# Kernel tuning notes

Hardware: AMD Instinct MI355X
Metric: run time of the kernel (lower is better)

The kernel has to match this reference:

```python
import jax, jax.numpy as jnp
import numpy as np

N = 100000          # atoms
E = 3200000         # edges (avg degree 32)
G = 2000            # molecules in batch
HID = 64            # hidden_channels == num_filters
NG = 50             # num_gaussians
CUTOFF = 10.0
LOG2 = float(np.log(2.0))


def ssp(x):
    # shifted softplus: softplus(x) - log(2)
    return jax.nn.softplus(x) - LOG2


def setup_inputs() -> dict:
    key = jax.random.key(0)
    ks = jax.random.split(key, 24)
    z = jax.random.randint(ks[0], (N,), 0, 100)
    pos = jax.random.uniform(ks[1], (N, 3), dtype=jnp.float32) * 5.0  # distances < cutoff
    batch = jnp.sort(jax.random.randint(ks[2], (N,), 0, G))
    edge_index = jax.random.randint(ks[3], (2, E), 0, N)

    def w(k, *shape):
        fan_in = shape[0]
        return jax.random.normal(k, shape, dtype=jnp.float32) / jnp.sqrt(jnp.float32(fan_in))

    emb = jax.random.normal(ks[4], (100, HID), dtype=jnp.float32)
    L = 3  # num_interactions; stack per-layer params on leading axis
    params = {
        'mlp_w1': w(ks[5], NG, HID)[None].repeat(L, 0) * 0 + jnp.stack([w(jax.random.fold_in(ks[5], i), NG, HID) for i in range(L)]),
        'mlp_b1': jnp.zeros((L, HID), jnp.float32),
        'mlp_w2': jnp.stack([w(jax.random.fold_in(ks[6], i), HID, HID) for i in range(L)]),
        'mlp_b2': jnp.zeros((L, HID), jnp.float32),
        'cf_lin1_w': jnp.stack([w(jax.random.fold_in(ks[7], i), HID, HID) for i in range(L)]),  # no bias
        'cf_lin2_w': jnp.stack([w(jax.random.fold_in(ks[8], i), HID, HID) for i in range(L)]),
        'cf_lin2_b': jnp.zeros((L, HID), jnp.float32),
        'int_lin_w': jnp.stack([w(jax.random.fold_in(ks[9], i), HID, HID) for i in range(L)]),
        'int_lin_b': jnp.zeros((L, HID), jnp.float32),
    }
    out_w1 = w(ks[10], HID, HID // 2)
    out_b1 = jnp.zeros((HID // 2,), jnp.float32)
    out_w2 = w(ks[11], HID // 2, 1)
    out_b2 = jnp.zeros((1,), jnp.float32)
    fin_w = w(ks[12], 1, 1)
    fin_b = jnp.zeros((1,), jnp.float32)
    return dict(z=z, pos=pos, batch=batch, edge_index=edge_index, emb=emb,
                out_w1=out_w1, out_b1=out_b1, out_w2=out_w2, out_b2=out_b2,
                fin_w=fin_w, fin_b=fin_b, **params)


def reference(z, pos, batch, edge_index, emb,
              mlp_w1, mlp_b1, mlp_w2, mlp_b2,
              cf_lin1_w, cf_lin2_w, cf_lin2_b,
              int_lin_w, int_lin_b,
              out_w1, out_b1, out_w2, out_b2, fin_w, fin_b):
    src, dst = edge_index[0], edge_index[1]
    h = emb[z]                                   # [N, 64]
    # edge distances
    d = jnp.linalg.norm(pos[src] - pos[dst], axis=-1)        # [E]
    # Gaussian smearing
    offsets = jnp.linspace(0.0, CUTOFF, NG, dtype=jnp.float32)
    delta = offsets[1] - offsets[0]
    coeff = -0.5 / (delta * delta)
    rbf = jnp.exp(coeff * (d[:, None] - offsets) ** 2)       # [E, 50]
    # cosine cutoff
    C = 0.5 * (jnp.cos(d * (jnp.pi / CUTOFF)) + 1.0)         # [E]

    L = mlp_w1.shape[0]
    for l in range(L):  # small fixed number of interaction blocks
        W = ssp(rbf @ mlp_w1[l] + mlp_b1[l]) @ mlp_w2[l] + mlp_b2[l]  # [E, 64]
        W = W * C[:, None]
        x = h @ cf_lin1_w[l]                                  # [N, 64]
        msg = x[src] * W                                      # [E, 64]
        agg = jax.ops.segment_sum(msg, dst, num_segments=N)   # [N, 64]
        x = agg @ cf_lin2_w[l] + cf_lin2_b[l]
        x = ssp(x)
        x = x @ int_lin_w[l] + int_lin_b[l]
        h = h + x

    h = ssp(h @ out_w1 + out_b1) @ out_w2 + out_b2            # [N, 1]
    out = jax.ops.segment_sum(h, batch, num_segments=G)       # [G, 1]
    return out @ fin_w + fin_b                                # trailing Linear(1,1)
```

## Files before the change

kernel.cpp:

```cpp
#include <hip/hip_runtime.h>
#include <hip/hip_fp16.h>
#include <cstdint>
#include <cstddef>

#define HIDC   64
#define NGAUSS 50
#define NLAYER 3
#define TGRID  8192
#define BSTRIDE 128
#define MAXBUCK 1024
#define CHUNK_E 6656
#define CUTOFF_F 10.0f
#define LOG2_C 0.69314718055994530942f

typedef _Float16 f16x8 __attribute__((ext_vector_type(8)));
typedef float f32x4 __attribute__((ext_vector_type(4)));
#define MFMA16(a, b, c) __builtin_amdgcn_mfma_f32_16x16x32_f16(a, b, c, 0, 0, 0)

__device__ __forceinline__ float sspf(float v) {
  return fmaxf(v, 0.0f) + log1pf(expf(-fabsf(v))) - LOG2_C;
}

__global__ __launch_bounds__(64) void build_table_k(
    const float* __restrict__ mlp_w1, const float* __restrict__ mlp_b1,
    const float* __restrict__ mlp_w2, const float* __restrict__ mlp_b2,
    __half* __restrict__ tabh) {
  int pid = blockIdx.x;
  int l = pid / TGRID;
  int g = pid - l * TGRID;
  int j = threadIdx.x;
  float d = (float)g * (CUTOFF_F / (float)(TGRID - 1));
  __shared__ float rbf_s[NGAUSS];
  __shared__ float hid_s[HIDC];
  const float delta = CUTOFF_F / (float)(NGAUSS - 1);
  const float coeff = -0.5f / (delta * delta);
  if (j < NGAUSS) {
    float t = d - (float)j * delta;
    rbf_s[j] = expf(coeff * t * t);
  }
  __syncthreads();
  const float* w1 = mlp_w1 + (size_t)l * NGAUSS * HIDC;
  float acc = mlp_b1[l * HIDC + j];
#pragma unroll
  for (int k = 0; k < NGAUSS; ++k) acc = fmaf(rbf_s[k], w1[k * HIDC + j], acc);
  hid_s[j] = sspf(acc);
  __syncthreads();
  const float* w2 = mlp_w2 + (size_t)l * HIDC * HIDC;
  float acc2 = mlp_b2[l * HIDC + j];
#pragma unroll
  for (int m = 0; m < HIDC; ++m) acc2 = fmaf(hid_s[m], w2[m * HIDC + j], acc2);
  float C = 0.5f * (cosf(d * (3.14159265358979323846f / CUTOFF_F)) + 1.0f);
  tabh[(size_t)pid * HIDC + j] = __float2half(acc2 * C);
}

__global__ __launch_bounds__(64) void pack_all_k(
    const float* __restrict__ cf1, const float* __restrict__ cf2,
    const float* __restrict__ intw, const float* __restrict__ ow1,
    __half* __restrict__ wpk) {
  int m = blockIdx.x;
  int lane = threadIdx.x;
  const float* src;
  int nc = 64;
  if (m < 3)      src = cf1 + (size_t)m * 4096;
  else if (m < 6) src = cf2 + (size_t)(m - 3) * 4096;
  else if (m < 9) src = intw + (size_t)(m - 6) * 4096;
  else          { src = ow1; nc = 32; }
  __half* dst = wpk + (size_t)m * 4096;
  for (int ct = 0; ct < nc / 16; ++ct)
    for (int kh = 0; kh < 2; ++kh)
      for (int j = 0; j < 8; ++j)
        dst[((ct * 2 + kh) * 64 + lane) * 8 + j] =
            __float2half(src[(kh * 32 + (lane >> 4) * 8 + j) * nc +
                             ct * 16 + (lane & 15)]);
}

__global__ __launch_bounds__(256) void chist_k(
    const int* __restrict__ edst, int* __restrict__ chunk_hist,
    int* __restrict__ bcnt, int E, int nbuck) {
  __shared__ int cnt[MAXBUCK];
  for (int i = threadIdx.x; i < MAXBUCK; i += 256) cnt[i] = 0;
  __syncthreads();
  int c = blockIdx.x;
  int e0 = c * CHUNK_E;
  int e1 = e0 + CHUNK_E; if (e1 > E) e1 = E;
  for (int e = e0 + threadIdx.x; e < e1; e += 256)
    atomicAdd(&cnt[edst[e] >> 7], 1);
  __syncthreads();
  for (int i = threadIdx.x; i < nbuck; i += 256) {
    int v = cnt[i];
    chunk_hist[c * MAXBUCK + i] = v;
    if (v) atomicAdd(&bcnt[i], v);
  }
}

__global__ __launch_bounds__(256) void bscan_k(
    const int* __restrict__ bcnt, int* __restrict__ boff, int nbuck) {
  __shared__ int sbuf[2][256];
  int tid = threadIdx.x;
  int base = tid * 4;
  int v0 = (base + 0 < nbuck) ? bcnt[base + 0] : 0;
  int v1 = (base + 1 < nbuck) ? bcnt[base + 1] : 0;
  int v2 = (base + 2 < nbuck) ? bcnt[base + 2] : 0;
  int v3 = (base + 3 < nbuck) ? bcnt[base + 3] : 0;
  int p0 = v0, p1 = p0 + v1, p2 = p1 + v2, p3 = p2 + v3;
  int pout = 0;
  sbuf[0][tid] = p3;
  __syncthreads();
  for (int off = 1; off < 256; off <<= 1) {
    int pin = pout; pout ^= 1;
    int v = sbuf[pin][tid];
    if (tid >= off) v += sbuf[pin][tid - off];
    sbuf[pout][tid] = v;
    __syncthreads();
  }
  int texc = sbuf[pout][tid] - p3;
  if (base + 0 < nbuck) boff[base + 0] = texc;
  if (base + 1 < nbuck) boff[base + 1] = texc + p0;
  if (base + 2 < nbuck) boff[base + 2] = texc + p1;
  if (base + 3 < nbuck) boff[base + 3] = texc + p2;
}

__global__ __launch_bounds__(256) void cbase_k(
    const int* __restrict__ chunk_hist, const int* __restrict__ boff,
    int* __restrict__ chunk_base, int nchunk) {
  __shared__ int sbuf[2][256];
  int b = blockIdx.x;
  int tid = threadIdx.x;
  int carry = 0;
  for (int t0 = 0; t0 < nchunk; t0 += 256) {
    int t = t0 + tid;
    int v = (t < nchunk) ? chunk_hist[(size_t)t * MAXBUCK + b] : 0;
    int pout = 0;
    sbuf[0][tid] = v;
    __syncthreads();
    for (int off = 1; off < 256; off <<= 1) {
      int pin = pout; pout ^= 1;
      int s = sbuf[pin][tid];
      if (tid >= off) s += sbuf[pin][tid - off];
      sbuf[pout][tid] = s;
      __syncthreads();
    }
    if (t < nchunk)
      chunk_base[(size_t)t * MAXBUCK + b] = boff[b] + carry + sbuf[pout][tid] - v;
    carry += sbuf[pout][255];
    __syncthreads();
  }
}

__global__ __launch_bounds__(256) void cstage_k(
    const int* __restrict__ ei, const float* __restrict__ pos,
    const int* __restrict__ chunk_hist, const int* __restrict__ chunk_base,
    int2* __restrict__ er, int E, int nbuck) {
  __shared__ int stage_a[CHUNK_E];
  __shared__ int stage_b[CHUNK_E];
  __shared__ int loff[MAXBUCK];
  __shared__ int lcur[MAXBUCK];
  __shared__ int sbuf[2][256];
  int c = blockIdx.x;
  int tid = threadIdx.x;
  const int* hrow = chunk_hist + (size_t)c * MAXBUCK;
  int base4 = tid * 4;
  int v0 = (base4 + 0 < nbuck) ? hrow[base4 + 0] : 0;
  int v1 = (base4 + 1 < nbuck) ? hrow[base4 + 1] : 0;
  int v2 = (base4 + 2 < nbuck) ? hrow[base4 + 2] : 0;
  int v3 = (base4 + 3 < nbuck) ? hrow[base4 + 3] : 0;
  int p0 = v0, p1 = p0 + v1, p2 = p1 + v2, p3 = p2 + v3;
  int pout = 0;
  sbuf[0][tid] = p3;
  __syncthreads();
  for (int off = 1; off < 256; off <<= 1) {
    int pin = pout; pout ^= 1;
    int v = sbuf[pin][tid];
    if (tid >= off) v += sbuf[pin][tid - off];
    sbuf[pout][tid] = v;
    __syncthreads();
  }
  int texc = sbuf[pout][tid] - p3;
  if (base4 + 0 < MAXBUCK) { loff[base4 + 0] = texc;      lcur[base4 + 0] = texc; }
  if (base4 + 1 < MAXBUCK) { loff[base4 + 1] = texc + p0; lcur[base4 + 1] = texc + p0; }
  if (base4 + 2 < MAXBUCK) { loff[base4 + 2] = texc + p1; lcur[base4 + 2] = texc + p1; }
  if (base4 + 3 < MAXBUCK) { loff[base4 + 3] = texc + p2; lcur[base4 + 3] = texc + p2; }
  __syncthreads();
  int e0 = c * CHUNK_E;
  int e1 = e0 + CHUNK_E; if (e1 > E) e1 = E;
  for (int e = e0 + tid; e < e1; e += 256) {
    int s = ei[e], t = ei[E + e];
    float dx = pos[3 * s + 0] - pos[3 * t + 0];
    float dy = pos[3 * s + 1] - pos[3 * t + 1];
    float dz = pos[3 * s + 2] - pos[3 * t + 2];
    float d = sqrtf(fmaf(dx, dx, fmaf(dy, dy, dz * dz)));
    float u = d * ((float)(TGRID - 1) / CUTOFF_F);
    int i0 = (int)(u + 0.5f);
    if (i0 > TGRID - 1) i0 = TGRID - 1;
    int b = t >> 7;
    int dl = t & 127;
    int p = atomicAdd(&lcur[b], 1);
    stage_a[p] = s | (dl << 20);
    stage_b[p] = i0 | (b << 13);
  }
  __syncthreads();
  int total = e1 - e0;
  for (int i = tid; i < total; i += 256) {
    int sb = stage_b[i];
    int b = sb >> 13;
    int gb = chunk_base[(size_t)c * MAXBUCK + b];
    er[gb + (i - loff[b])] = make_int2(stage_a[i], sb & 0x1FFF);
  }
}

__global__ __launch_bounds__(256) void bsort_k(
    const int* __restrict__ boff, const int* __restrict__ bcnt,
    const int2* __restrict__ er, int* __restrict__ er2,
    int* __restrict__ rs, int n) {
  __shared__ int dcnt[BSTRIDE];
  __shared__ int lcur[BSTRIDE];
  __shared__ int sc[2][BSTRIDE];
  int b = blockIdx.x;
  int node0 = b << 7;
  int nn = n - node0; if (nn > BSTRIDE) nn = BSTRIDE;
  int tid = threadIdx.x;
  if (tid < BSTRIDE) dcnt[tid] = 0;
  __syncthreads();
  int base = boff[b];
  int cnt = bcnt[b];
  for (int r = tid; r < cnt; r += 256)
    atomicAdd(&dcnt[(unsigned)er[base + r].x >> 20], 1);
  __syncthreads();
  int pout = 0;
  if (tid < BSTRIDE) sc[0][tid] = dcnt[tid];
  __syncthreads();
  for (int off = 1; off < BSTRIDE; off <<= 1) {
    int pin = pout; pout ^= 1;
    if (tid < BSTRIDE) {
      int v = sc[pin][tid];
      if (tid >= off) v += sc[pin][tid - off];
      sc[pout][tid] = v;
    }
    __syncthreads();
  }
  if (tid < BSTRIDE) {
    int start = base + sc[pout][tid] - dcnt[tid];
    lcur[tid] = start;
    if (tid < nn) rs[node0 + tid] = start;
  }
  if (tid == 0 && b == gridDim.x - 1) rs[n] = base + cnt;
  __syncthreads();
  for (int r = tid; r < cnt; r += 256) {
    int2 rec = er[base + r];
    int dl = (unsigned)rec.x >> 20;
    int p = atomicAdd(&lcur[dl], 1);
    er2[p] = (rec.x & 0x1FFFF) | (rec.y << 17);
  }
}

__global__ __launch_bounds__(256) void init_h_k(
    const int* __restrict__ z, const float* __restrict__ emb,
    float* __restrict__ h, __half* __restrict__ h16, int n64) {
  int i = blockIdx.x * blockDim.x + threadIdx.x;
  if (i >= n64) return;
  float v = emb[(z[i >> 6] << 6) | (i & 63)];
  h[i] = v;
  h16[i] = __float2half(v);
}


#define LOADB(Wpk) \
  const f16x8* Bp = (const f16x8*)(Wpk); \
  const f16x8 b00 = Bp[0 * 64 + lane], b01 = Bp[1 * 64 + lane]; \
  const f16x8 b10 = Bp[2 * 64 + lane], b11 = Bp[3 * 64 + lane]; \
  const f16x8 b20 = Bp[4 * 64 + lane], b21 = Bp[5 * 64 + lane]; \
  const f16x8 b30 = Bp[6 * 64 + lane], b31 = Bp[7 * 64 + lane];

#define GEMM_PRO \
  const int lane = threadIdx.x & 63; \
  const int r = lane & 15, g = lane >> 4; \
  const int wid = __builtin_amdgcn_readfirstlane( \
      (int)((blockIdx.x * 256 + threadIdx.x) >> 6)); \
  const int nwv = (int)(gridDim.x << 2); \
  const f32x4 z4 = {0.f, 0.f, 0.f, 0.f};

#define GEMM_BODY(xin) \
  int arow = t * 16 + r; if (arow >= n) arow = n - 1; \
  const f16x8* Ap = (const f16x8*)((xin) + ((size_t)arow << 6)); \
  const f16x8 a0 = Ap[g], a1 = Ap[4 + g]; \
  f32x4 c0 = MFMA16(a0, b00, z4); c0 = MFMA16(a1, b01, c0); \
  f32x4 c1 = MFMA16(a0, b10, z4); c1 = MFMA16(a1, b11, c1); \
  f32x4 c2 = MFMA16(a0, b20, z4); c2 = MFMA16(a1, b21, c2); \
  f32x4 c3 = MFMA16(a0, b30, z4); c3 = MFMA16(a1, b31, c3);

__global__ __launch_bounds__(256, 4) void lin16_k(
    const __half* __restrict__ xin, const __half* __restrict__ wpk,
    __half* __restrict__ xout, int ntiles, int n) {
  GEMM_PRO
  LOADB(wpk)
  for (int t = wid; t < ntiles; t += nwv) {
    GEMM_BODY(xin)
    const int nb = t * 16 + (g << 2);
#pragma unroll
    for (int q = 0; q < 4; ++q) {
      const int node = nb + q;
      if (node < n) {
        __half* o = xout + ((size_t)node << 6) + r;
        o[0]  = __float2half(c0[q]);
        o[16] = __float2half(c1[q]);
        o[32] = __float2half(c2[q]);
        o[48] = __float2half(c3[q]);
      }
    }
  }
}

__global__ __launch_bounds__(256, 4) void up1_16_k(
    const __half* __restrict__ xin, const __half* __restrict__ wpk,
    const float* __restrict__ b2, __half* __restrict__ xout,
    int ntiles, int n) {
  GEMM_PRO
  LOADB(wpk)
  const float bb0 = b2[r], bb1 = b2[16 + r], bb2 = b2[32 + r], bb3 = b2[48 + r];
  for (int t = wid; t < ntiles; t += nwv) {
    GEMM_BODY(xin)
    const int nb = t * 16 + (g << 2);
#pragma unroll
    for (int q = 0; q < 4; ++q) {
      const int node = nb + q;
      if (node < n) {
        __half* o = xout + ((size_t)node << 6) + r;
        o[0]  = __float2half(sspf(c0[q] + bb0));
        o[16] = __float2half(sspf(c1[q] + bb1));
        o[32] = __float2half(sspf(c2[q] + bb2));
        o[48] = __float2half(sspf(c3[q] + bb3));
      }
    }
  }
}

__global__ __launch_bounds__(256, 4) void up2_16_k(
    const __half* __restrict__ xin, const __half* __restrict__ wpk,
    const float* __restrict__ b3, float* __restrict__ h,
    __half* __restrict__ h16, int ntiles, int n) {
  GEMM_PRO
  LOADB(wpk)
  const float bb0 = b3[r], bb1 = b3[16 + r], bb2 = b3[32 + r], bb3 = b3[48 + r];
  for (int t = wid; t < ntiles; t += nwv) {
    GEMM_BODY(xin)
    const int nb = t * 16 + (g << 2);
#pragma unroll
    for (int q = 0; q < 4; ++q) {
      const int node = nb + q;
      if (node < n) {
        const size_t idx = ((size_t)node << 6) + r;
        float n0 = h[idx +  0] + c0[q] + bb0;
        float n1 = h[idx + 16] + c1[q] + bb1;
        float n2 = h[idx + 32] + c2[q] + bb2;
        float n3 = h[idx + 48] + c3[q] + bb3;
        h[idx +  0] = n0; h16[idx +  0] = __float2half(n0);
        h[idx + 16] = n1; h16[idx + 16] = __float2half(n1);
        h[idx + 32] = n2; h16[idx + 32] = __float2half(n2);
        h[idx + 48] = n3; h16[idx + 48] = __float2half(n3);
      }
    }
  }
}

__global__ __launch_bounds__(256, 4) void outm16_k(
    const __half* __restrict__ h16, const int* __restrict__ batch,
    const __half* __restrict__ wpk, const float* __restrict__ ob1,
    const float* __restrict__ ow2, const float* __restrict__ ob2,
    float* __restrict__ outg, int ntiles, int n) {
  GEMM_PRO
  const f16x8* Bp = (const f16x8*)(wpk);
  const f16x8 b00 = Bp[0 * 64 + lane], b01 = Bp[1 * 64 + lane];
  const f16x8 b10 = Bp[2 * 64 + lane], b11 = Bp[3 * 64 + lane];
  const float b1a = ob1[r], b1b = ob1[16 + r];
  const float w2a = ow2[r], w2b = ow2[16 + r];
  const float b2o = ob2[0];
  for (int t = wid; t < ntiles; t += nwv) {
    int arow = t * 16 + r; if (arow >= n) arow = n - 1;
    const f16x8* Ap = (const f16x8*)(h16 + ((size_t)arow << 6));
    const f16x8 a0 = Ap[g], a1 = Ap[4 + g];
    f32x4 c0 = MFMA16(a0, b00, z4); c0 = MFMA16(a1, b01, c0);
    f32x4 c1 = MFMA16(a0, b10, z4); c1 = MFMA16(a1, b11, c1);
    float v0 = sspf(c0[0] + b1a) * w2a + sspf(c1[0] + b1b) * w2b;
    float v1 = sspf(c0[1] + b1a) * w2a + sspf(c1[1] + b1b) * w2b;
    float v2 = sspf(c0[2] + b1a) * w2a + sspf(c1[2] + b1b) * w2b;
    float v3 = sspf(c0[3] + b1a) * w2a + sspf(c1[3] + b1b) * w2b;
#pragma unroll
    for (int off = 1; off < 16; off <<= 1) {
      v0 += __shfl_xor(v0, off);
      v1 += __shfl_xor(v1, off);
      v2 += __shfl_xor(v2, off);
      v3 += __shfl_xor(v3, off);
    }
    if (r == 0) {
      const int nb = t * 16 + (g << 2);
      if (nb + 0 < n) unsafeAtomicAdd(&outg[batch[nb + 0]], v0 + b2o);
      if (nb + 1 < n) unsafeAtomicAdd(&outg[batch[nb + 1]], v1 + b2o);
      if (nb + 2 < n) unsafeAtomicAdd(&outg[batch[nb + 2]], v2 + b2o);
      if (nb + 3 < n) unsafeAtomicAdd(&outg[batch[nb + 3]], v3 + b2o);
    }
  }
}

__global__ __launch_bounds__(256) void gather_k(
    const int* __restrict__ rs, const int* __restrict__ er,
    const __half* __restrict__ tabh, const __half* __restrict__ x,
    __half* __restrict__ aggh, int n) {
  int j = threadIdx.x & 63;
  int node = (blockIdx.x * 256 + threadIdx.x) >> 6;
  if (node >= n) return;
  int beg = __builtin_amdgcn_readfirstlane(rs[node]);
  int end = __builtin_amdgcn_readfirstlane(rs[node + 1]);
  float acc = 0.0f;
  int k = beg;
  for (; k + 8 <= end; k += 8) {
    int r0 = er[k + 0];
    int r1 = er[k + 1];
    int r2 = er[k + 2];
    int r3 = er[k + 3];
    int r4 = er[k + 4];
    int r5 = er[k + 5];
    int r6 = er[k + 6];
    int r7 = er[k + 7];
    float t0 = __half2float(tabh[(((size_t)((unsigned)r0 >> 17)) << 6) + j]);
    float t1 = __half2float(tabh[(((size_t)((unsigned)r1 >> 17)) << 6) + j]);
    float t2 = __half2float(tabh[(((size_t)((unsigned)r2 >> 17)) << 6) + j]);
    float t3 = __half2float(tabh[(((size_t)((unsigned)r3 >> 17)) << 6) + j]);
    float t4 = __half2float(tabh[(((size_t)((unsigned)r4 >> 17)) << 6) + j]);
    float t5 = __half2float(tabh[(((size_t)((unsigned)r5 >> 17)) << 6) + j]);
    float t6 = __half2float(tabh[(((size_t)((unsigned)r6 >> 17)) << 6) + j]);
    float t7 = __half2float(tabh[(((size_t)((unsigned)r7 >> 17)) << 6) + j]);
    float x0 = __half2float(x[((size_t)(r0 & 0x1FFFF) << 6) + j]);
    float x1 = __half2float(x[((size_t)(r1 & 0x1FFFF) << 6) + j]);
    float x2 = __half2float(x[((size_t)(r2 & 0x1FFFF) << 6) + j]);
    float x3 = __half2float(x[((size_t)(r3 & 0x1FFFF) << 6) + j]);
    float x4 = __half2float(x[((size_t)(r4 & 0x1FFFF) << 6) + j]);
    float x5 = __half2float(x[((size_t)(r5 & 0x1FFFF) << 6) + j]);
    float x6 = __half2float(x[((size_t)(r6 & 0x1FFFF) << 6) + j]);
    float x7 = __half2float(x[((size_t)(r7 & 0x1FFFF) << 6) + j]);
    acc = fmaf(x0, t0, acc);
    acc = fmaf(x1, t1, acc);
    acc = fmaf(x2, t2, acc);
    acc = fmaf(x3, t3, acc);
    acc = fmaf(x4, t4, acc);
    acc = fmaf(x5, t5, acc);
    acc = fmaf(x6, t6, acc);
    acc = fmaf(x7, t7, acc);
  }
  for (; k + 4 <= end; k += 4) {
    int r0 = er[k + 0];
    int r1 = er[k + 1];
    int r2 = er[k + 2];
    int r3 = er[k + 3];
    float t0 = __half2float(tabh[(((size_t)((unsigned)r0 >> 17)) << 6) + j]);
    float t1 = __half2float(tabh[(((size_t)((unsigned)r1 >> 17)) << 6) + j]);
    float t2 = __half2float(tabh[(((size_t)((unsigned)r2 >> 17)) << 6) + j]);
    float t3 = __half2float(tabh[(((size_t)((unsigned)r3 >> 17)) << 6) + j]);
    float x0 = __half2float(x[((size_t)(r0 & 0x1FFFF) << 6) + j]);
    float x1 = __half2float(x[((size_t)(r1 & 0x1FFFF) << 6) + j]);
    float x2 = __half2float(x[((size_t)(r2 & 0x1FFFF) << 6) + j]);
    float x3 = __half2float(x[((size_t)(r3 & 0x1FFFF) << 6) + j]);
    acc = fmaf(x0, t0, acc);
    acc = fmaf(x1, t1, acc);
    acc = fmaf(x2, t2, acc);
    acc = fmaf(x3, t3, acc);
  }
  for (; k < end; ++k) {
    int r = er[k];
    float t = __half2float(tabh[(((size_t)((unsigned)r >> 17)) << 6) + j]);
    float xv = __half2float(x[((size_t)(r & 0x1FFFF) << 6) + j]);
    acc = fmaf(xv, t, acc);
  }
  aggh[((size_t)node << 6) + j] = __float2half(acc);
}

__global__ __launch_bounds__(256) void final_k(
    const float* __restrict__ outg, const float* __restrict__ fw,
    const float* __restrict__ fb, float* __restrict__ out, int g) {
  int i = blockIdx.x * blockDim.x + threadIdx.x;
  if (i < g) out[i] = fmaf(outg[i], fw[0], fb[0]);
}

extern "C" void kernel_launch(void* const* d_in, const int* in_sizes, int n_in,
                              void* d_out, int out_size, void* d_ws, size_t ws_size,
                              hipStream_t stream) {
  const int*   z      = (const int*)d_in[0];
  const float* pos    = (const float*)d_in[1];
  const int*   batch  = (const int*)d_in[2];
  const int*   ei     = (const int*)d_in[3];
  const float* emb    = (const float*)d_in[4];
  const float* out_w1 = (const float*)d_in[5];
  const float* out_b1 = (const float*)d_in[6];
  const float* out_w2 = (const float*)d_in[7];
  const float* out_b2 = (const float*)d_in[8];
  const float* fin_w  = (const float*)d_in[9];
  const float* fin_b  = (const float*)d_in[10];
  const float* mlp_w1 = (const float*)d_in[11];
  const float* mlp_b1 = (const float*)d_in[12];
  const float* mlp_w2 = (const float*)d_in[13];
  const float* mlp_b2 = (const float*)d_in[14];
  const float* cf1    = (const float*)d_in[15];
  const float* cf2    = (const float*)d_in[16];
  const float* cf2b   = (const float*)d_in[17];
  const float* intw   = (const float*)d_in[18];
  const float* intb   = (const float*)d_in[19];

  const int N = in_sizes[0];
  const int E = in_sizes[3] / 2;
  const int G = out_size;
  const int NBUCK = (N + BSTRIDE - 1) / BSTRIDE;
  const int NCHUNK = (E + CHUNK_E - 1) / CHUNK_E;
  const int NTILES = (N + 15) / 16;
  const int GB = (NTILES + 3) / 4;

  char* wsb = (char*)d_ws;
  size_t off = 0;
  auto alloc = [&](size_t bytes) { char* p = wsb + off; off += (bytes + 255) & ~(size_t)255; return p; };
  float*   h     = (float*)alloc((size_t)N * HIDC * sizeof(float));
  __half*  h16   = (__half*)alloc((size_t)N * HIDC * sizeof(__half));
  __half*  x     = (__half*)alloc((size_t)N * HIDC * sizeof(__half));
  __half*  aggh  = (__half*)alloc((size_t)N * HIDC * sizeof(__half));
  __half*  t16   = (__half*)alloc((size_t)N * HIDC * sizeof(__half));
  __half*  tabh  = (__half*)alloc((size_t)NLAYER * TGRID * HIDC * sizeof(__half));
  __half*  wpk   = (__half*)alloc((size_t)10 * 4096 * sizeof(__half));
  int2*    er    = (int2*)alloc((size_t)E * sizeof(int2));
  int*     er2   = (int*)alloc((size_t)E * sizeof(int));
  int*     rs    = (int*)alloc((size_t)(N + 1) * sizeof(int));
  int*     bcnt  = (int*)alloc((size_t)MAXBUCK * sizeof(int));
  int*     boff  = (int*)alloc((size_t)MAXBUCK * sizeof(int));
  int*     chist = (int*)alloc((size_t)NCHUNK * MAXBUCK * sizeof(int));
  int*     cbase = (int*)alloc((size_t)NCHUNK * MAXBUCK * sizeof(int));
  float*   outg  = (float*)alloc((size_t)G * sizeof(float));

  build_table_k<<<dim3(NLAYER * TGRID), dim3(64), 0, stream>>>(
      mlp_w1, mlp_b1, mlp_w2, mlp_b2, tabh);
  pack_all_k<<<dim3(10), dim3(64), 0, stream>>>(cf1, cf2, intw, out_w1, wpk);
  hipMemsetAsync(outg, 0, (size_t)G * sizeof(float), stream);
  hipMemsetAsync(bcnt, 0, (size_t)MAXBUCK * sizeof(int), stream);
  chist_k<<<dim3(NCHUNK), dim3(256), 0, stream>>>(ei + E, chist, bcnt, E, NBUCK);
  bscan_k<<<dim3(1), dim3(256), 0, stream>>>(bcnt, boff, NBUCK);
  cbase_k<<<dim3(NBUCK), dim3(256), 0, stream>>>(chist, boff, cbase, NCHUNK);
  cstage_k<<<dim3(NCHUNK), dim3(256), 0, stream>>>(
      ei, pos, chist, cbase, er, E, NBUCK);
  bsort_k<<<dim3(NBUCK), dim3(256), 0, stream>>>(boff, bcnt, er, er2, rs, N);
  init_h_k<<<dim3((N * HIDC + 255) / 256), dim3(256), 0, stream>>>(
      z, emb, h, h16, N * HIDC);

  const int gather_blocks = (N + 3) / 4;
  for (int l = 0; l < NLAYER; ++l) {
    lin16_k<<<dim3(GB), dim3(256), 0, stream>>>(
        h16, wpk + (size_t)l * 4096, x, NTILES, N);
    gather_k<<<dim3(gather_blocks), dim3(256), 0, stream>>>(
        rs, er2, tabh + (size_t)l * TGRID * HIDC, x, aggh, N);
    up1_16_k<<<dim3(GB), dim3(256), 0, stream>>>(
        aggh, wpk + (size_t)(3 + l) * 4096, cf2b + l * HIDC, t16, NTILES, N);
    up2_16_k<<<dim3(GB), dim3(256), 0, stream>>>(
        t16, wpk + (size_t)(6 + l) * 4096, intb + l * HIDC, h, h16, NTILES, N);
  }

  outm16_k<<<dim3(GB), dim3(256), 0, stream>>>(
      h16, batch, wpk + (size_t)9 * 4096, out_b1, out_w2, out_b2, outg, NTILES, N);
  final_k<<<dim3((G + 255) / 256), dim3(256), 0, stream>>>(
      outg, fin_w, fin_b, (float*)d_out, G);
}
```

Measured before the change: 611.9 us.

## Fuse per-layer node GEMMs into one kernel and embedding init with first linear

Chains the three per-node GEMMs of each layer (cf_lin2 with ssp, int_lin with residual, and the next layer's cf_lin1) inside one kernel, handing the 16x64 tile between MFMA stages through a per-wave LDS transpose. The embedding lookup is merged with the first cf_lin1. This removes the t16 intermediate buffer, several N×64 global round-trips and multiple launches per layer. Separately, cstage_k now runs 512 threads with a 2-per-thread scan that reuses stage_a as scratch. The cost is more weight registers per thread (launch bounds lowered to 2 blocks) and extra LDS traffic.

```diff
diff --git a/kernel.cpp b/kernel.cpp
--- a/kernel.cpp
+++ b/kernel.cpp
@@ -147,7 +147,7 @@
   }
 }
 
-__global__ __launch_bounds__(256) void cstage_k(
+__global__ __launch_bounds__(512) void cstage_k(
     const int* __restrict__ ei, const float* __restrict__ pos,
     const int* __restrict__ chunk_hist, const int* __restrict__ chunk_base,
     int2* __restrict__ er, int E, int nbuck) {
@@ -155,35 +155,31 @@
   __shared__ int stage_b[CHUNK_E];
   __shared__ int loff[MAXBUCK];
   __shared__ int lcur[MAXBUCK];
-  __shared__ int sbuf[2][256];
   int c = blockIdx.x;
   int tid = threadIdx.x;
   const int* hrow = chunk_hist + (size_t)c * MAXBUCK;
-  int base4 = tid * 4;
-  int v0 = (base4 + 0 < nbuck) ? hrow[base4 + 0] : 0;
-  int v1 = (base4 + 1 < nbuck) ? hrow[base4 + 1] : 0;
-  int v2 = (base4 + 2 < nbuck) ? hrow[base4 + 2] : 0;
-  int v3 = (base4 + 3 < nbuck) ? hrow[base4 + 3] : 0;
-  int p0 = v0, p1 = p0 + v1, p2 = p1 + v2, p3 = p2 + v3;
+  int b0 = tid * 2;
+  int v0 = (b0     < nbuck) ? hrow[b0]     : 0;
+  int v1 = (b0 + 1 < nbuck) ? hrow[b0 + 1] : 0;
+  int p1 = v0 + v1;
+  int (*sb)[512] = (int (*)[512])stage_a;
   int pout = 0;
-  sbuf[0][tid] = p3;
-  __syncthreads();
-  for (int off = 1; off < 256; off <<= 1) {
+  sb[0][tid] = p1;
+  __syncthreads();
+  for (int off = 1; off < 512; off <<= 1) {
     int pin = pout; pout ^= 1;
-    int v = sbuf[pin][tid];
-    if (tid >= off) v += sbuf[pin][tid - off];
-    sbuf[pout][tid] = v;
+    int v = sb[pin][tid];
+    if (tid >= off) v += sb[pin][tid - off];
+    sb[pout][tid] = v;
     __syncthreads();
   }
-  int texc = sbuf[pout][tid] - p3;
-  if (base4 + 0 < MAXBUCK) { loff[base4 + 0] = texc;      lcur[base4 + 0] = texc; }
-  if (base4 + 1 < MAXBUCK) { loff[base4 + 1] = texc + p0; lcur[base4 + 1] = texc + p0; }
-  if (base4 + 2 < MAXBUCK) { loff[base4 + 2] = texc + p1; lcur[base4 + 2] = texc + p1; }
-  if (base4 + 3 < MAXBUCK) { loff[base4 + 3] = texc + p2; lcur[base4 + 3] = texc + p2; }
+  int texc = sb[pout][tid] - p1;
+  loff[b0] = texc;          lcur[b0] = texc;
+  loff[b0 + 1] = texc + v0; lcur[b0 + 1] = texc + v0;
   __syncthreads();
   int e0 = c * CHUNK_E;
   int e1 = e0 + CHUNK_E; if (e1 > E) e1 = E;
-  for (int e = e0 + tid; e < e1; e += 256) {
+  for (int e = e0 + tid; e < e1; e += 512) {
     int s = ei[e], t = ei[E + e];
     float dx = pos[3 * s + 0] - pos[3 * t + 0];
     float dy = pos[3 * s + 1] - pos[3 * t + 1];
@@ -200,11 +196,11 @@
   }
   __syncthreads();
   int total = e1 - e0;
-  for (int i = tid; i < total; i += 256) {
-    int sb = stage_b[i];
-    int b = sb >> 13;
+  for (int i = tid; i < total; i += 512) {
+    int sbv = stage_b[i];
+    int b = sbv >> 13;
     int gb = chunk_base[(size_t)c * MAXBUCK + b];
-    er[gb + (i - loff[b])] = make_int2(stage_a[i], sb & 0x1FFF);
+    er[gb + (i - loff[b])] = make_int2(stage_a[i], sbv & 0x1FFF);
   }
 }
 
@@ -253,23 +249,13 @@
   }
 }
 
-__global__ __launch_bounds__(256) void init_h_k(
-    const int* __restrict__ z, const float* __restrict__ emb,
-    float* __restrict__ h, __half* __restrict__ h16, int n64) {
-  int i = blockIdx.x * blockDim.x + threadIdx.x;
-  if (i >= n64) return;
-  float v = emb[(z[i >> 6] << 6) | (i & 63)];
-  h[i] = v;
-  h16[i] = __float2half(v);
-}
-
-
-#define LOADB(Wpk) \
-  const f16x8* Bp = (const f16x8*)(Wpk); \
-  const f16x8 b00 = Bp[0 * 64 + lane], b01 = Bp[1 * 64 + lane]; \
-  const f16x8 b10 = Bp[2 * 64 + lane], b11 = Bp[3 * 64 + lane]; \
-  const f16x8 b20 = Bp[4 * 64 + lane], b21 = Bp[5 * 64 + lane]; \
-  const f16x8 b30 = Bp[6 * 64 + lane], b31 = Bp[7 * 64 + lane];
+
+#define LOADB_P(P, Wpk) \
+  const f16x8* P##p = (const f16x8*)(Wpk); \
+  const f16x8 P##00 = P##p[0 * 64 + lane], P##01 = P##p[1 * 64 + lane]; \
+  const f16x8 P##10 = P##p[2 * 64 + lane], P##11 = P##p[3 * 64 + lane]; \
+  const f16x8 P##20 = P##p[4 * 64 + lane], P##21 = P##p[5 * 64 + lane]; \
+  const f16x8 P##30 = P##p[6 * 64 + lane], P##31 = P##p[7 * 64 + lane];
 
 #define GEMM_PRO \
   const int lane = threadIdx.x & 63; \
@@ -279,28 +265,50 @@
   const int nwv = (int)(gridDim.x << 2); \
   const f32x4 z4 = {0.f, 0.f, 0.f, 0.f};
 
-#define GEMM_BODY(xin) \
-  int arow = t * 16 + r; if (arow >= n) arow = n - 1; \
-  const f16x8* Ap = (const f16x8*)((xin) + ((size_t)arow << 6)); \
-  const f16x8 a0 = Ap[g], a1 = Ap[4 + g]; \
-  f32x4 c0 = MFMA16(a0, b00, z4); c0 = MFMA16(a1, b01, c0); \
-  f32x4 c1 = MFMA16(a0, b10, z4); c1 = MFMA16(a1, b11, c1); \
-  f32x4 c2 = MFMA16(a0, b20, z4); c2 = MFMA16(a1, b21, c2); \
-  f32x4 c3 = MFMA16(a0, b30, z4); c3 = MFMA16(a1, b31, c3);
-
-__global__ __launch_bounds__(256, 4) void lin16_k(
-    const __half* __restrict__ xin, const __half* __restrict__ wpk,
-    __half* __restrict__ xout, int ntiles, int n) {
+#define MFMA8(P, a0, a1, c0, c1, c2, c3) \
+  c0 = MFMA16(a0, P##00, z4); c0 = MFMA16(a1, P##01, c0); \
+  c1 = MFMA16(a0, P##10, z4); c1 = MFMA16(a1, P##11, c1); \
+  c2 = MFMA16(a0, P##20, z4); c2 = MFMA16(a1, P##21, c2); \
+  c3 = MFMA16(a0, P##30, z4); c3 = MFMA16(a1, P##31, c3);
+
+__global__ __launch_bounds__(256, 2) void init_lin_k(
+    const int* __restrict__ z, const float* __restrict__ emb,
+    const __half* __restrict__ wpk, float* __restrict__ h,
+    __half* __restrict__ h16, __half* __restrict__ x, int ntiles, int n) {
   GEMM_PRO
-  LOADB(wpk)
+  LOADB_P(B, wpk)
   for (int t = wid; t < ntiles; t += nwv) {
-    GEMM_BODY(xin)
+    int node = t * 16 + r;
+    int nodec = node < n ? node : n - 1;
+    const int zi = z[nodec];
+    const float4* ep = (const float4*)(emb + ((size_t)zi << 6));
+    float4 ea = ep[g * 2], eb = ep[g * 2 + 1];
+    float4 ec = ep[8 + g * 2], ed = ep[8 + g * 2 + 1];
+    f16x8 a0, a1;
+    a0[0] = (_Float16)ea.x; a0[1] = (_Float16)ea.y;
+    a0[2] = (_Float16)ea.z; a0[3] = (_Float16)ea.w;
+    a0[4] = (_Float16)eb.x; a0[5] = (_Float16)eb.y;
+    a0[6] = (_Float16)eb.z; a0[7] = (_Float16)eb.w;
+    a1[0] = (_Float16)ec.x; a1[1] = (_Float16)ec.y;
+    a1[2] = (_Float16)ec.z; a1[3] = (_Float16)ec.w;
+    a1[4] = (_Float16)ed.x; a1[5] = (_Float16)ed.y;
+    a1[6] = (_Float16)ed.z; a1[7] = (_Float16)ed.w;
+    if (node < n) {
+      float4* hp = (float4*)(h + ((size_t)node << 6) + g * 8);
+      hp[0] = ea; hp[1] = eb;
+      float4* hp2 = (float4*)(h + ((size_t)node << 6) + 32 + g * 8);
+      hp2[0] = ec; hp2[1] = ed;
+      *(f16x8*)(h16 + ((size_t)node << 6) + g * 8) = a0;
+      *(f16x8*)(h16 + ((size_t)node << 6) + 32 + g * 8) = a1;
+    }
+    f32x4 c0, c1, c2, c3;
+    MFMA8(B, a0, a1, c0, c1, c2, c3)
     const int nb = t * 16 + (g << 2);
 #pragma unroll
     for (int q = 0; q < 4; ++q) {
-      const int node = nb + q;
-      if (node < n) {
-        __half* o = xout + ((size_t)node << 6) + r;
+      const int nq = nb + q;
+      if (nq < n) {
+        __half* o = x + ((size_t)nq << 6) + r;
         o[0]  = __float2half(c0[q]);
         o[16] = __float2half(c1[q]);
         o[32] = __float2half(c2[q]);
@@ -310,53 +318,118 @@
   }
 }
 
-__global__ __launch_bounds__(256, 4) void up1_16_k(
-    const __half* __restrict__ xin, const __half* __restrict__ wpk,
-    const float* __restrict__ b2, __half* __restrict__ xout,
-    int ntiles, int n) {
-  GEMM_PRO
-  LOADB(wpk)
-  const float bb0 = b2[r], bb1 = b2[16 + r], bb2 = b2[32 + r], bb3 = b2[48 + r];
-  for (int t = wid; t < ntiles; t += nwv) {
-    GEMM_BODY(xin)
-    const int nb = t * 16 + (g << 2);
-#pragma unroll
-    for (int q = 0; q < 4; ++q) {
-      const int node = nb + q;
-      if (node < n) {
-        __half* o = xout + ((size_t)node << 6) + r;
-        o[0]  = __float2half(sspf(c0[q] + bb0));
-        o[16] = __float2half(sspf(c1[q] + bb1));
-        o[32] = __float2half(sspf(c2[q] + bb2));
-        o[48] = __float2half(sspf(c3[q] + bb3));
-      }
-    }
-  }
-}
-
-__global__ __launch_bounds__(256, 4) void up2_16_k(
-    const __half* __restrict__ xin, const __half* __restrict__ wpk,
+__global__ __launch_bounds__(256, 2) void upd0_k(
+    const __half* __restrict__ aggh, const __half* __restrict__ wpk2,
+    const float* __restrict__ b2, const __half* __restrict__ wpk3,
     const float* __restrict__ b3, float* __restrict__ h,
     __half* __restrict__ h16, int ntiles, int n) {
+  __shared__ _Float16 lt[4][16][72];
   GEMM_PRO
-  LOADB(wpk)
-  const float bb0 = b3[r], bb1 = b3[16 + r], bb2 = b3[32 + r], bb3 = b3[48 + r];
+  const int wslot = threadIdx.x >> 6;
+  _Float16 (*T)[72] = lt[wslot];
+  LOADB_P(B2, wpk2)
+  LOADB_P(B3, wpk3)
+  const float q2a = b2[r], q2b = b2[16 + r], q2c = b2[32 + r], q2d = b2[48 + r];
+  const float q3a = b3[r], q3b = b3[16 + r], q3c = b3[32 + r], q3d = b3[48 + r];
   for (int t = wid; t < ntiles; t += nwv) {
-    GEMM_BODY(xin)
+    int arow = t * 16 + r; if (arow >= n) arow = n - 1;
+    const f16x8* Ap = (const f16x8*)(aggh + ((size_t)arow << 6));
+    const f16x8 a0 = Ap[g], a1 = Ap[4 + g];
+    f32x4 c0, c1, c2, c3;
+    MFMA8(B2, a0, a1, c0, c1, c2, c3)
+#pragma unroll
+    for (int q = 0; q < 4; ++q) {
+      T[g * 4 + q][r]      = (_Float16)sspf(c0[q] + q2a);
+      T[g * 4 + q][16 + r] = (_Float16)sspf(c1[q] + q2b);
+      T[g * 4 + q][32 + r] = (_Float16)sspf(c2[q] + q2c);
+      T[g * 4 + q][48 + r] = (_Float16)sspf(c3[q] + q2d);
+    }
+    const f16x8 t0 = *(const f16x8*)&T[r][g * 8];
+    const f16x8 t1 = *(const f16x8*)&T[r][32 + g * 8];
+    MFMA8(B3, t0, t1, c0, c1, c2, c3)
     const int nb = t * 16 + (g << 2);
 #pragma unroll
     for (int q = 0; q < 4; ++q) {
-      const int node = nb + q;
-      if (node < n) {
-        const size_t idx = ((size_t)node << 6) + r;
-        float n0 = h[idx +  0] + c0[q] + bb0;
-        float n1 = h[idx + 16] + c1[q] + bb1;
-        float n2 = h[idx + 32] + c2[q] + bb2;
-        float n3 = h[idx + 48] + c3[q] + bb3;
+      const int nq = nb + q;
+      if (nq < n) {
+        const size_t idx = ((size_t)nq << 6) + r;
+        float n0 = h[idx +  0] + c0[q] + q3a;
+        float n1 = h[idx + 16] + c1[q] + q3b;
+        float n2 = h[idx + 32] + c2[q] + q3c;
+        float n3 = h[idx + 48] + c3[q] + q3d;
         h[idx +  0] = n0; h16[idx +  0] = __float2half(n0);
         h[idx + 16] = n1; h16[idx + 16] = __float2half(n1);
         h[idx + 32] = n2; h16[idx + 32] = __float2half(n2);
         h[idx + 48] = n3; h16[idx + 48] = __float2half(n3);
+      }
+    }
+  }
+}
+
+__global__ __launch_bounds__(256, 2) void upd1_k(
+    const __half* __restrict__ aggh, const __half* __restrict__ wpk2,
+    const float* __restrict__ b2, const __half* __restrict__ wpk3,
+    const float* __restrict__ b3, float* __restrict__ h,
+    __half* __restrict__ h16, const __half* __restrict__ wpkC,
+    __half* __restrict__ x, int ntiles, int n) {
+  __shared__ _Float16 lt[4][16][72];
+  GEMM_PRO
+  const int wslot = threadIdx.x >> 6;
+  _Float16 (*T)[72] = lt[wslot];
+  LOADB_P(B2, wpk2)
+  LOADB_P(B3, wpk3)
+  LOADB_P(BC, wpkC)
+  const float q2a = b2[r], q2b = b2[16 + r], q2c = b2[32 + r], q2d = b2[48 + r];
+  const float q3a = b3[r], q3b = b3[16 + r], q3c = b3[32 + r], q3d = b3[48 + r];
+  for (int t = wid; t < ntiles; t += nwv) {
+    int arow = t * 16 + r; if (arow >= n) arow = n - 1;
+    const f16x8* Ap = (const f16x8*)(aggh + ((size_t)arow << 6));
+    const f16x8 a0 = Ap[g], a1 = Ap[4 + g];
+    f32x4 c0, c1, c2, c3;
+    MFMA8(B2, a0, a1, c0, c1, c2, c3)
+#pragma unroll
+    for (int q = 0; q < 4; ++q) {
+      T[g * 4 + q][r]      = (_Float16)sspf(c0[q] + q2a);
+      T[g * 4 + q][16 + r] = (_Float16)sspf(c1[q] + q2b);
+      T[g * 4 + q][32 + r] = (_Float16)sspf(c2[q] + q2c);
+      T[g * 4 + q][48 + r] = (_Float16)sspf(c3[q] + q2d);
+    }
+    const f16x8 t0 = *(const f16x8*)&T[r][g * 8];
+    const f16x8 t1 = *(const f16x8*)&T[r][32 + g * 8];
+    MFMA8(B3, t0, t1, c0, c1, c2, c3)
+    const int nb = t * 16 + (g << 2);
+#pragma unroll
+    for (int q = 0; q < 4; ++q) {
+      const int nq = nb + q;
+      float n0 = 0.f, n1 = 0.f, n2 = 0.f, n3 = 0.f;
+      if (nq < n) {
+        const size_t idx = ((size_t)nq << 6) + r;
+        n0 = h[idx +  0] + c0[q] + q3a;
+        n1 = h[idx + 16] + c1[q] + q3b;
+        n2 = h[idx + 32] + c2[q] + q3c;
+        n3 = h[idx + 48] + c3[q] + q3d;
+        h[idx +  0] = n0; h16[idx +  0] = __float2half(n0);
+        h[idx + 16] = n1; h16[idx + 16] = __float2half(n1);
+        h[idx + 32] = n2; h16[idx + 32] = __float2half(n2);
+        h[idx + 48] = n3; h16[idx + 48] = __float2half(n3);
+      }
+      T[g * 4 + q][r]      = (_Float16)n0;
+      T[g * 4 + q][16 + r] = (_Float16)n1;
+      T[g * 4 + q][32 + r] = (_Float16)n2;
+      T[g * 4 + q][48 + r] = (_Float16)n3;
+    }
+    const f16x8 h0 = *(const f16x8*)&T[r][g * 8];
+    const f16x8 h1 = *(const f16x8*)&T[r][32 + g * 8];
+    MFMA8(BC, h0, h1, c0, c1, c2, c3)
+#pragma unroll
+    for (int q = 0; q < 4; ++q) {
+      const int nq = nb + q;
+      if (nq < n) {
+        __half* o = x + ((size_t)nq << 6) + r;
+        o[0]  = __float2half(c0[q]);
+        o[16] = __float2half(c1[q]);
+        o[32] = __float2half(c2[q]);
+        o[48] = __float2half(c3[q]);
       }
     }
   }
@@ -519,7 +592,6 @@
   __half*  h16   = (__half*)alloc((size_t)N * HIDC * sizeof(__half));
   __half*  x     = (__half*)alloc((size_t)N * HIDC * sizeof(__half));
   __half*  aggh  = (__half*)alloc((size_t)N * HIDC * sizeof(__half));
-  __half*  t16   = (__half*)alloc((size_t)N * HIDC * sizeof(__half));
   __half*  tabh  = (__half*)alloc((size_t)NLAYER * TGRID * HIDC * sizeof(__half));
   __half*  wpk   = (__half*)alloc((size_t)10 * 4096 * sizeof(__half));
   int2*    er    = (int2*)alloc((size_t)E * sizeof(int2));
@@ -534,27 +606,31 @@
   build_table_k<<<dim3(NLAYER * TGRID), dim3(64), 0, stream>>>(
       mlp_w1, mlp_b1, mlp_w2, mlp_b2, tabh);
   pack_all_k<<<dim3(10), dim3(64), 0, stream>>>(cf1, cf2, intw, out_w1, wpk);
-  hipMemsetAsync(outg, 0, (size_t)G * sizeof(float), stream);
-  hipMemsetAsync(bcnt, 0, (size_t)MAXBUCK * sizeof(int), stream);
+  (void)hipMemsetAsync(outg, 0, (size_t)G * sizeof(float), stream);
+  (void)hipMemsetAsync(bcnt, 0, (size_t)MAXBUCK * sizeof(int), stream);
   chist_k<<<dim3(NCHUNK), dim3(256), 0, stream>>>(ei + E, chist, bcnt, E, NBUCK);
   bscan_k<<<dim3(1), dim3(256), 0, stream>>>(bcnt, boff, NBUCK);
   cbase_k<<<dim3(NBUCK), dim3(256), 0, stream>>>(chist, boff, cbase, NCHUNK);
-  cstage_k<<<dim3(NCHUNK), dim3(256), 0, stream>>>(
+  cstage_k<<<dim3(NCHUNK), dim3(512), 0, stream>>>(
       ei, pos, chist, cbase, er, E, NBUCK);
   bsort_k<<<dim3(NBUCK), dim3(256), 0, stream>>>(boff, bcnt, er, er2, rs, N);
-  init_h_k<<<dim3((N * HIDC + 255) / 256), dim3(256), 0, stream>>>(
-      z, emb, h, h16, N * HIDC);
+  init_lin_k<<<dim3(GB), dim3(256), 0, stream>>>(
+      z, emb, wpk, h, h16, x, NTILES, N);
 
   const int gather_blocks = (N + 3) / 4;
   for (int l = 0; l < NLAYER; ++l) {
-    lin16_k<<<dim3(GB), dim3(256), 0, stream>>>(
-        h16, wpk + (size_t)l * 4096, x, NTILES, N);
     gather_k<<<dim3(gather_blocks), dim3(256), 0, stream>>>(
         rs, er2, tabh + (size_t)l * TGRID * HIDC, x, aggh, N);
-    up1_16_k<<<dim3(GB), dim3(256), 0, stream>>>(
-        aggh, wpk + (size_t)(3 + l) * 4096, cf2b + l * HIDC, t16, NTILES, N);
-    up2_16_k<<<dim3(GB), dim3(256), 0, stream>>>(
-        t16, wpk + (size_t)(6 + l) * 4096, intb + l * HIDC, h, h16, NTILES, N);
+    if (l < NLAYER - 1) {
+      upd1_k<<<dim3(GB), dim3(256), 0, stream>>>(
+          aggh, wpk + (size_t)(3 + l) * 4096, cf2b + l * HIDC,
+          wpk + (size_t)(6 + l) * 4096, intb + l * HIDC, h, h16,
+          wpk + (size_t)(l + 1) * 4096, x, NTILES, N);
+    } else {
+      upd0_k<<<dim3(GB), dim3(256), 0, stream>>>(
+          aggh, wpk + (size_t)(3 + l) * 4096, cf2b + l * HIDC,
+          wpk + (size_t)(6 + l) * 4096, intb + l * HIDC, h, h16, NTILES, N);
+    }
   }
 
   outm16_k<<<dim3(GB), dim3(256), 0, stream>>>(
```

After: 553.8 us. -9.5%, faster.
